# Optimization experiments

Hardware: AMD Instinct MI355X
Metric: run time of the kernel (lower is better)

## Reference

```python
import jax, jax.numpy as jnp
import numpy as np

B, N, F_IN, E, TOPK = 64, 1024, 64, 128, 32
NEG_SLOPE = 0.2  # GAT leaky-relu slope


def setup_inputs() -> dict:
    key = jax.random.key(0)
    ks = jax.random.split(key, 7)
    x = jax.random.normal(ks[0], (B, N, F_IN), dtype=jnp.float32)
    emb = jax.random.normal(ks[1], (N, E), dtype=jnp.float32)            # nn.Embedding table
    W_fe = jax.random.normal(ks[2], (F_IN, E), dtype=jnp.float32) / np.sqrt(F_IN).astype(np.float32)
    a_src = jax.random.normal(ks[3], (2 * E,), dtype=jnp.float32) * 0.05
    a_dst = jax.random.normal(ks[4], (2 * E,), dtype=jnp.float32) * 0.05
    lin_W = jax.random.normal(ks[5], (E, 1), dtype=jnp.float32) / np.sqrt(E).astype(np.float32)
    lin_b = jnp.zeros((1,), dtype=jnp.float32)
    return {"x": x, "emb": emb, "W_fe": W_fe, "a_src": a_src, "a_dst": a_dst,
            "lin_W": lin_W, "lin_b": lin_b}


def reference(x, emb, W_fe, a_src, a_dst, lin_W, lin_b):
    b, n, _ = x.shape
    e_dim = emb.shape[-1]
    # --- cosine-similarity topk graph construction (shared across batch) ---
    norm = jnp.linalg.norm(emb, axis=-1, keepdims=True)                  # [N,1]
    sim = (emb @ emb.T) / (norm @ norm.T)                                # [N,N]
    idx = jax.lax.top_k(sim, TOPK)[1]                                    # [N,K] int32 neighbor (target) nodes
    # --- graph attention feature extraction ---
    h = jnp.einsum('bnf,fe->bne', x, W_fe)                               # [B,N,E] projected node features
    g = jnp.concatenate([h, jnp.broadcast_to(emb, (b, n, e_dim))], -1)   # [B,N,2E] feat || embedding
    e_s = g @ a_src                                                      # [B,N] source attention term
    e_d = g @ a_dst                                                      # [B,N] target attention term
    # edges: source i repeated TOPK times -> targets idx[i]; softmax over each node's K neighbors
    scores = jax.nn.leaky_relu(e_s[:, :, None] + e_d[:, idx], NEG_SLOPE)  # [B,N,K]
    alpha = jax.nn.softmax(scores, axis=-1)                              # [B,N,K]
    h_dst = h[:, idx, :]                                                 # [B,N,K,E] gathered neighbor feats
    out = jnp.einsum('bnk,bnke->bne', alpha, h_dst)                      # aggregate messages
    out = jax.nn.relu(out)
    # --- linear readout ---
    y = out @ lin_W + lin_b                                              # [B,N,1]
    return y[..., 0]                                                     # [B,N]
```

## Files before the change

kernel.cpp:

```cpp
#include <hip/hip_runtime.h>
#include <math.h>

#define BB 64
#define NN 1024
#define F_IN 64
#define EE 128
#define TOPK 32
#define NEG_SLOPE 0.2f

typedef unsigned int uint;
typedef unsigned short ushort;
typedef unsigned long long ull;
typedef __attribute__((ext_vector_type(8))) short short8;
typedef __attribute__((ext_vector_type(4))) float f32x4;

static __device__ __forceinline__ uint f2bf(float f) {
  const uint x = __float_as_uint(f);
  return (x + 0x7fffu + ((x >> 16) & 1u)) >> 16;
}
static __device__ __forceinline__ float bf_lo(uint u) {
  return __uint_as_float(u << 16);
}
static __device__ __forceinline__ float bf_hi_raw(uint u) {
  return __uint_as_float(u);
}
static __device__ __forceinline__ uint fmono(float f) {
  uint u = __float_as_uint(f);
  return (u & 0x80000000u) ? ~u : (u | 0x80000000u);
}
static __device__ __forceinline__ ull umax64(ull a, ull b) {
  return a > b ? a : b;
}
static __device__ __forceinline__ ull umin64(ull a, ull b) {
  return a < b ? a : b;
}
static __device__ __forceinline__ ull shfl_xor64(ull v, int mask) {
  const uint lo = __shfl_xor((uint)v, mask);
  const uint hi = __shfl_xor((uint)(v >> 32), mask);
  return ((ull)hi << 32) | lo;
}

__global__ __launch_bounds__(256) void k2a_sim(
    const float* __restrict__ emb, const float* __restrict__ a_src,
    const float* __restrict__ a_dst, const float* __restrict__ W_fe,
    uint* __restrict__ keys, float* __restrict__ u_src,
    float* __restrict__ u_dst, ushort* __restrict__ wt) {
  __shared__ __align__(16) float ei[8][132];
  __shared__ __align__(16) float ej[64][132];
  const int t = threadIdx.x, wid = t >> 6, lane = t & 63;
  const int i0 = (blockIdx.x >> 2) * 8;
  const int jbase = (blockIdx.x & 3) * 256;

  if ((blockIdx.x & 3) == 0) {
    const int row = i0 + 2 * wid + (lane >> 5);
    const int ll = lane & 31;
    const float* er = emb + (size_t)row * EE;
    float us = 0.f, ud = 0.f;
#pragma unroll
    for (int c0 = 0; c0 < EE; c0 += 32) {
      const int c = c0 + ll;
      const float e = er[c];
      us += e * a_src[EE + c];
      ud += e * a_dst[EE + c];
    }
#pragma unroll
    for (int o = 1; o <= 16; o <<= 1) {
      us += __shfl_xor(us, o);
      ud += __shfl_xor(ud, o);
    }
    if (ll == 0) {
      u_src[row] = us;
      u_dst[row] = ud;
    }
  } else if ((blockIdx.x & 3) == 1 && (blockIdx.x >> 2) < 32) {
    const int g = (blockIdx.x >> 2) * 256 + t;
    const int n = g >> 6, k = g & 63;
    wt[g] = (ushort)f2bf(W_fe[k * EE + n]);
  }

  {
    const int r = t >> 5, c4 = t & 31;
    const float4 v = *(const float4*)&emb[(size_t)(i0 + r) * EE + c4 * 4];
    *(float4*)&ei[r][c4 * 4] = v;
  }

  const int ia = i0 + wid * 2;

  for (int ch = 0; ch < 4; ++ch) {
    const int j0 = jbase + ch * 64;
#pragma unroll
    for (int p = 0; p < 8; ++p) {
      const int g = p * 256 + t;
      const int r = g >> 5, c4 = g & 31;
      const float4 v = *(const float4*)&emb[(size_t)(j0 + r) * EE + c4 * 4];
      *(float4*)&ej[r][c4 * 4] = v;
    }
    __syncthreads();

    float a0 = 0.f, a1 = 0.f, sq = 0.f;
#pragma unroll 8
    for (int d4 = 0; d4 < 32; ++d4) {
      const float4 e = *(const float4*)&ej[lane][4 * d4];
      const float4 wa = *(const float4*)&ei[wid * 2][4 * d4];
      const float4 wb = *(const float4*)&ei[wid * 2 + 1][4 * d4];
      a0 += e.x * wa.x + e.y * wa.y + e.z * wa.z + e.w * wa.w;
      a1 += e.x * wb.x + e.y * wb.y + e.z * wb.z + e.w * wb.w;
      sq += e.x * e.x + e.y * e.y + e.z * e.z + e.w * e.w;
    }
    const int jg = j0 + lane;
    const float rj = rsqrtf(sq);
    keys[(size_t)ia * NN + jg] = fmono(a0 * rj);
    keys[(size_t)(ia + 1) * NN + jg] = fmono(a1 * rj);
    __syncthreads();
  }
}

__global__ __launch_bounds__(256) void k23(
    const uint* __restrict__ keys, int* __restrict__ idx_out,
    const float* __restrict__ x, const ushort* __restrict__ wt,
    const float* __restrict__ a_src, const float* __restrict__ a_dst,
    const float* __restrict__ u_src, const float* __restrict__ u_dst,
    uint* __restrict__ h2, float* __restrict__ es, float* __restrict__ ed) {
  __shared__ ull cand[128];
  const int t = threadIdx.x, wid = t >> 6, lane = t & 63;

  if (blockIdx.x < NN) {
    const int row = blockIdx.x;

    const int jb = wid * 256 + lane * 4;
    const uint4 kv = *(const uint4*)&keys[(size_t)row * NN + jb];
    ull xr[4];
    xr[0] = ((ull)kv.x << 32) | (uint)(jb + 0);
    xr[1] = ((ull)kv.y << 32) | (uint)(jb + 1);
    xr[2] = ((ull)kv.z << 32) | (uint)(jb + 2);
    xr[3] = ((ull)kv.w << 32) | (uint)(jb + 3);

#pragma unroll
    for (int k = 2; k <= 256; k <<= 1) {
#pragma unroll
      for (int d = 128; d >= 1; d >>= 1) {
        if (d > (k >> 1)) continue;
        if (d >= 4) {
          const int pl = d >> 2;
          const bool lower = (lane & pl) == 0;
#pragma unroll
          for (int r = 0; r < 4; ++r) {
            const ull o = shfl_xor64(xr[r], pl);
            const bool desc = (((lane * 4 + r) & k) == 0);
            const bool keepmax = (desc == lower);
            xr[r] = keepmax ? umax64(xr[r], o) : umin64(xr[r], o);
          }
        } else if (d == 2) {
#pragma unroll
          for (int r = 0; r < 2; ++r) {
            const bool desc = (((lane * 4 + r) & k) == 0);
            const ull hi = umax64(xr[r], xr[r + 2]);
            const ull lo = umin64(xr[r], xr[r + 2]);
            xr[r] = desc ? hi : lo;
            xr[r + 2] = desc ? lo : hi;
          }
        } else {
#pragma unroll
          for (int r = 0; r < 4; r += 2) {
            const bool desc = (((lane * 4 + r) & k) == 0);
            const ull hi = umax64(xr[r], xr[r + 1]);
            const ull lo = umin64(xr[r], xr[r + 1]);
            xr[r] = desc ? hi : lo;
            xr[r + 1] = desc ? lo : hi;
          }
        }
      }
    }
    if (lane < 8) {
#pragma unroll
      for (int r = 0; r < 4; ++r) cand[wid * 32 + lane * 4 + r] = xr[r];
    }
    __syncthreads();

    if (wid < 2) {
      const int base = wid * 64;
      ull v = (lane < 32) ? cand[base + lane] : cand[base + 95 - lane];
#pragma unroll
      for (int d = 32; d >= 1; d >>= 1) {
        const ull o = shfl_xor64(v, d);
        v = ((lane & d) == 0) ? umax64(v, o) : umin64(v, o);
      }
      if (lane < 32) cand[base + lane] = v;
    }
    __syncthreads();

    if (wid == 0) {
      ull v = (lane < 32) ? cand[lane] : cand[127 - lane];
#pragma unroll
      for (int d = 32; d >= 1; d >>= 1) {
        const ull o = shfl_xor64(v, d);
        v = ((lane & d) == 0) ? umax64(v, o) : umin64(v, o);
      }
      if (lane < 32) idx_out[(size_t)row * TOPK + lane] = (int)(v & 1023u);
    }
  } else {
    const int row0 = (blockIdx.x - NN) * 64;
    const int nn = lane & 15, quad = lane >> 4;
    const int row0w = row0 + wid * 16;

    short8 af[2];
#pragma unroll
    for (int s = 0; s < 2; ++s) {
      const float* xr2 = x + (size_t)(row0w + nn) * F_IN + s * 32 + quad * 8;
      const float4 v0 = *(const float4*)&xr2[0];
      const float4 v1 = *(const float4*)&xr2[4];
      af[s][0] = (short)f2bf(v0.x);
      af[s][1] = (short)f2bf(v0.y);
      af[s][2] = (short)f2bf(v0.z);
      af[s][3] = (short)f2bf(v0.w);
      af[s][4] = (short)f2bf(v1.x);
      af[s][5] = (short)f2bf(v1.y);
      af[s][6] = (short)f2bf(v1.z);
      af[s][7] = (short)f2bf(v1.w);
    }

    f32x4 acc[8];
#pragma unroll
    for (int T = 0; T < 8; ++T) acc[T] = (f32x4){0.f, 0.f, 0.f, 0.f};

#pragma unroll
    for (int T = 0; T < 8; ++T) {
#pragma unroll
      for (int s = 0; s < 2; ++s) {
        const short8 bf =
            *(const short8*)&wt[(T * 16 + nn) * F_IN + s * 32 + quad * 8];
        acc[T] =
            __builtin_amdgcn_mfma_f32_16x16x32_bf16(af[s], bf, acc[T], 0, 0, 0);
      }
    }

    const int growbase = row0w + quad * 4;
#pragma unroll
    for (int reg = 0; reg < 4; ++reg) {
      uint* hr = h2 + (size_t)(growbase + reg) * 64 + nn;
#pragma unroll
      for (int T4 = 0; T4 < 4; ++T4) {
        hr[T4 * 16] =
            f2bf(acc[2 * T4][reg]) | (f2bf(acc[2 * T4 + 1][reg]) << 16);
      }
    }
    float ae[8], de[8];
#pragma unroll
    for (int T = 0; T < 8; ++T) {
      ae[T] = a_src[T * 16 + nn];
      de[T] = a_dst[T * 16 + nn];
    }
#pragma unroll
    for (int reg = 0; reg < 4; ++reg) {
      float ps = 0.f, pd = 0.f;
#pragma unroll
      for (int T = 0; T < 8; ++T) {
        ps += acc[T][reg] * ae[T];
        pd += acc[T][reg] * de[T];
      }
#pragma unroll
      for (int o = 1; o <= 8; o <<= 1) {
        ps += __shfl_xor(ps, o);
        pd += __shfl_xor(pd, o);
      }
      if (nn == 0) {
        const int grow = growbase + reg;
        const int node = grow & (NN - 1);
        es[grow] = ps + u_src[node];
        ed[grow] = pd + u_dst[node];
      }
    }
  }
}

__global__ __launch_bounds__(256) void k4_attn(
    const uint* __restrict__ h2, const float* __restrict__ es,
    const float* __restrict__ ed, const int* __restrict__ idx,
    const float* __restrict__ lin_W, const float* __restrict__ lin_b,
    float* __restrict__ y) {
  const int t = threadIdx.x, wid = t >> 6, lane = t & 63;
  const int blk = blockIdx.x;
  const int xcd = blk & 7, x = blk >> 3;
  const int b = xcd * 8 + (x >> 6);
  const int q = lane >> 4, ll = lane & 15;
  const int n = (x & 63) * 16 + wid * 4 + q;
  const int pbase = q * 64;

  const float* edb = ed + (size_t)b * NN;
  const float* esb = es + (size_t)b * NN;
  const char* hb = (const char*)(h2 + (size_t)b * NN * 64);

  const int j0 = idx[n * TOPK + ll];
  const int j1 = idx[n * TOPK + 16 + ll];
  const int off0 = j0 << 8, off1 = j1 << 8;
  int offA[16], offB[16];
#pragma unroll
  for (int k = 0; k < 16; ++k) {
    offA[k] = __builtin_amdgcn_ds_bpermute(pbase + k * 4, off0);
    offB[k] = __builtin_amdgcn_ds_bpermute(pbase + k * 4, off1);
  }
  uint4 tvA[16];
#pragma unroll
  for (int k = 0; k < 16; ++k)
    tvA[k] = *(const uint4*)(hb + ((uint)offA[k] + ll * 16));
  uint4 tvB[16];
#pragma unroll
  for (int k = 0; k < 16; ++k)
    tvB[k] = *(const uint4*)(hb + ((uint)offB[k] + ll * 16));

  const float esv = esb[n];
  float s0 = esv + edb[j0];
  float s1 = esv + edb[j1];
  s0 = s0 > 0.f ? s0 : NEG_SLOPE * s0;
  s1 = s1 > 0.f ? s1 : NEG_SLOPE * s1;
  const float p0 = __expf(s0);
  const float p1 = __expf(s1);
  float dsum = p0 + p1;
#pragma unroll
  for (int o = 1; o <= 8; o <<= 1) dsum += __shfl_xor(dsum, o);
  const float rs = 1.0f / dsum;
  const float w0 = p0 * rs, w1 = p1 * rs;
  float wkA[16], wkB[16];
#pragma unroll
  for (int k = 0; k < 16; ++k) {
    wkA[k] = __uint_as_float(
        __builtin_amdgcn_ds_bpermute(pbase + k * 4, __float_as_uint(w0)));
    wkB[k] = __uint_as_float(
        __builtin_amdgcn_ds_bpermute(pbase + k * 4, __float_as_uint(w1)));
  }

  float lwlo[4], lwhi[4];
#pragma unroll
  for (int i = 0; i < 4; ++i) {
    const int c = 4 * ll + i;
    const int t4 = c >> 4, nn2 = c & 15;
    lwlo[i] = lin_W[t4 * 32 + nn2];
    lwhi[i] = lin_W[t4 * 32 + 16 + nn2];
  }
  const float bias = lin_b[0];

  float acc[8];
#pragma unroll
  for (int i = 0; i < 8; i++) acc[i] = 0.f;
#pragma unroll
  for (int k = 0; k < 16; ++k) {
    const float ak = wkA[k];
    const uint4 u = tvA[k];
    acc[0] += ak * bf_lo(u.x);
    acc[1] += ak * bf_hi_raw(u.x);
    acc[2] += ak * bf_lo(u.y);
    acc[3] += ak * bf_hi_raw(u.y);
    acc[4] += ak * bf_lo(u.z);
    acc[5] += ak * bf_hi_raw(u.z);
    acc[6] += ak * bf_lo(u.w);
    acc[7] += ak * bf_hi_raw(u.w);
  }
#pragma unroll
  for (int k = 0; k < 16; ++k) {
    const float ak = wkB[k];
    const uint4 u = tvB[k];
    acc[0] += ak * bf_lo(u.x);
    acc[1] += ak * bf_hi_raw(u.x);
    acc[2] += ak * bf_lo(u.y);
    acc[3] += ak * bf_hi_raw(u.y);
    acc[4] += ak * bf_lo(u.z);
    acc[5] += ak * bf_hi_raw(u.z);
    acc[6] += ak * bf_lo(u.w);
    acc[7] += ak * bf_hi_raw(u.w);
  }
  float r = 0.f;
#pragma unroll
  for (int i = 0; i < 4; ++i) {
    const float a0 = acc[2 * i] > 0.f ? acc[2 * i] : 0.f;
    const float a1 = acc[2 * i + 1] > 0.f ? acc[2 * i + 1] : 0.f;
    r += a0 * lwlo[i] + a1 * lwhi[i];
  }
#pragma unroll
  for (int o = 1; o <= 8; o <<= 1) r += __shfl_xor(r, o);
  if (ll == 0) y[(size_t)b * NN + n] = r + bias;
}

extern "C" void kernel_launch(void* const* d_in, const int* in_sizes, int n_in,
                              void* d_out, int out_size, void* d_ws,
                              size_t ws_size, hipStream_t stream) {
  const float* x = (const float*)d_in[0];
  const float* emb = (const float*)d_in[1];
  const float* W_fe = (const float*)d_in[2];
  const float* a_src = (const float*)d_in[3];
  const float* a_dst = (const float*)d_in[4];
  const float* lin_W = (const float*)d_in[5];
  const float* lin_b = (const float*)d_in[6];
  float* y = (float*)d_out;

  char* ws = (char*)d_ws;
  float* u_src = (float*)(ws + 4096);
  float* u_dst = (float*)(ws + 8192);
  int* idx = (int*)(ws + 16384);
  float* es = (float*)(ws + 147456);
  float* ed = (float*)(ws + 409600);
  uint* h2 = (uint*)(ws + 671744);
  uint* keys = (uint*)(ws + 17448960);
  ushort* wt = (ushort*)(ws + 21643264);

  k2a_sim<<<512, 256, 0, stream>>>(emb, a_src, a_dst, W_fe, keys, u_src,
                                   u_dst, wt);
  k23<<<2048, 256, 0, stream>>>(keys, idx, x, wt, a_src, a_dst, u_src, u_dst,
                                h2, es, ed);
  k4_attn<<<4096, 256, 0, stream>>>(h2, es, ed, idx, lin_W, lin_b, y);
}
```

Before: 131.2 us.

## Stage neighbor offsets/weights in LDS and double-buffer gathers in attention kernel

Replaces the ds_bpermute broadcast of neighbor offsets and softmax weights with a per-node LDS staging array holding (offset, unnormalized exp) pairs. The 32 neighbor-row gathers are split into four groups of eight and double-buffered so loads overlap the FMA accumulation. Softmax normalization is deferred: the exp sum is accumulated in the loop and applied once after ReLU and the readout dot product, which is valid because the scale is positive. It also adds a launch_bounds occupancy hint of 3 blocks, cutting register pressure from 32 live uint4 values to 16. The LDS writes and reads happen within the same wavefront with no explicit barrier, which relies on in-order wave execution.

```diff
diff --git a/kernel.cpp b/kernel.cpp
--- a/kernel.cpp
+++ b/kernel.cpp
@@ -273,61 +273,39 @@
   }
 }
 
-__global__ __launch_bounds__(256) void k4_attn(
+__global__ __launch_bounds__(256, 3) void k4_attn(
     const uint* __restrict__ h2, const float* __restrict__ es,
     const float* __restrict__ ed, const int* __restrict__ idx,
     const float* __restrict__ lin_W, const float* __restrict__ lin_b,
     float* __restrict__ y) {
+  __shared__ uint2 pairs[16 * 34 + 2];
   const int t = threadIdx.x, wid = t >> 6, lane = t & 63;
   const int blk = blockIdx.x;
-  const int xcd = blk & 7, x = blk >> 3;
-  const int b = xcd * 8 + (x >> 6);
+  const int xcd = blk & 7, xx = blk >> 3;
+  const int b = xcd * 8 + (xx >> 6);
   const int q = lane >> 4, ll = lane & 15;
-  const int n = (x & 63) * 16 + wid * 4 + q;
-  const int pbase = q * 64;
+  const int n = (xx & 63) * 16 + wid * 4 + q;
+  uint2* const pr = pairs + (wid * 4 + q) * 34;
 
   const float* edb = ed + (size_t)b * NN;
-  const float* esb = es + (size_t)b * NN;
   const char* hb = (const char*)(h2 + (size_t)b * NN * 64);
 
   const int j0 = idx[n * TOPK + ll];
   const int j1 = idx[n * TOPK + 16 + ll];
-  const int off0 = j0 << 8, off1 = j1 << 8;
-  int offA[16], offB[16];
-#pragma unroll
-  for (int k = 0; k < 16; ++k) {
-    offA[k] = __builtin_amdgcn_ds_bpermute(pbase + k * 4, off0);
-    offB[k] = __builtin_amdgcn_ds_bpermute(pbase + k * 4, off1);
-  }
-  uint4 tvA[16];
-#pragma unroll
-  for (int k = 0; k < 16; ++k)
-    tvA[k] = *(const uint4*)(hb + ((uint)offA[k] + ll * 16));
-  uint4 tvB[16];
-#pragma unroll
-  for (int k = 0; k < 16; ++k)
-    tvB[k] = *(const uint4*)(hb + ((uint)offB[k] + ll * 16));
-
-  const float esv = esb[n];
+  const float esv = es[(size_t)b * NN + n];
   float s0 = esv + edb[j0];
   float s1 = esv + edb[j1];
   s0 = s0 > 0.f ? s0 : NEG_SLOPE * s0;
   s1 = s1 > 0.f ? s1 : NEG_SLOPE * s1;
   const float p0 = __expf(s0);
   const float p1 = __expf(s1);
-  float dsum = p0 + p1;
-#pragma unroll
-  for (int o = 1; o <= 8; o <<= 1) dsum += __shfl_xor(dsum, o);
-  const float rs = 1.0f / dsum;
-  const float w0 = p0 * rs, w1 = p1 * rs;
-  float wkA[16], wkB[16];
-#pragma unroll
-  for (int k = 0; k < 16; ++k) {
-    wkA[k] = __uint_as_float(
-        __builtin_amdgcn_ds_bpermute(pbase + k * 4, __float_as_uint(w0)));
-    wkB[k] = __uint_as_float(
-        __builtin_amdgcn_ds_bpermute(pbase + k * 4, __float_as_uint(w1)));
-  }
+  uint2 st0, st1;
+  st0.x = (uint)(j0 << 8);
+  st0.y = __float_as_uint(p0);
+  st1.x = (uint)(j1 << 8);
+  st1.y = __float_as_uint(p1);
+  pr[ll] = st0;
+  pr[16 + ll] = st1;
 
   float lwlo[4], lwhi[4];
 #pragma unroll
@@ -339,35 +317,50 @@
   }
   const float bias = lin_b[0];
 
+  float w[32];
   float acc[8];
 #pragma unroll
-  for (int i = 0; i < 8; i++) acc[i] = 0.f;
-#pragma unroll
-  for (int k = 0; k < 16; ++k) {
-    const float ak = wkA[k];
-    const uint4 u = tvA[k];
-    acc[0] += ak * bf_lo(u.x);
-    acc[1] += ak * bf_hi_raw(u.x);
-    acc[2] += ak * bf_lo(u.y);
-    acc[3] += ak * bf_hi_raw(u.y);
-    acc[4] += ak * bf_lo(u.z);
-    acc[5] += ak * bf_hi_raw(u.z);
-    acc[6] += ak * bf_lo(u.w);
-    acc[7] += ak * bf_hi_raw(u.w);
-  }
-#pragma unroll
-  for (int k = 0; k < 16; ++k) {
-    const float ak = wkB[k];
-    const uint4 u = tvB[k];
-    acc[0] += ak * bf_lo(u.x);
-    acc[1] += ak * bf_hi_raw(u.x);
-    acc[2] += ak * bf_lo(u.y);
-    acc[3] += ak * bf_hi_raw(u.y);
-    acc[4] += ak * bf_lo(u.z);
-    acc[5] += ak * bf_hi_raw(u.z);
-    acc[6] += ak * bf_lo(u.w);
-    acc[7] += ak * bf_hi_raw(u.w);
-  }
+  for (int i = 0; i < 8; ++i) acc[i] = 0.f;
+  float dsum = 0.f;
+  uint4 tvA[8], tvB[8];
+
+#define LOADG(g, TV)                                                \
+  {                                                                 \
+    _Pragma("unroll") for (int k = 0; k < 8; ++k) {                 \
+      const uint2 pw = pr[(g) * 8 + k];                             \
+      w[(g) * 8 + k] = __uint_as_float(pw.y);                       \
+      TV[k] = *(const uint4*)(hb + (pw.x + (uint)(ll * 16)));       \
+    }                                                               \
+  }
+#define CONSG(g, TV)                                \
+  {                                                 \
+    _Pragma("unroll") for (int k = 0; k < 8; ++k) { \
+      const float wk = w[(g) * 8 + k];              \
+      dsum += wk;                                   \
+      const uint4 u = TV[k];                        \
+      acc[0] += wk * bf_lo(u.x);                    \
+      acc[1] += wk * bf_hi_raw(u.x);                \
+      acc[2] += wk * bf_lo(u.y);                    \
+      acc[3] += wk * bf_hi_raw(u.y);                \
+      acc[4] += wk * bf_lo(u.z);                    \
+      acc[5] += wk * bf_hi_raw(u.z);                \
+      acc[6] += wk * bf_lo(u.w);                    \
+      acc[7] += wk * bf_hi_raw(u.w);                \
+    }                                               \
+  }
+
+  LOADG(0, tvA)
+  LOADG(1, tvB)
+  CONSG(0, tvA)
+  LOADG(2, tvA)
+  CONSG(1, tvB)
+  LOADG(3, tvB)
+  CONSG(2, tvA)
+  CONSG(3, tvB)
+#undef LOADG
+#undef CONSG
+
+  const float rs = 1.0f / dsum;
   float r = 0.f;
 #pragma unroll
   for (int i = 0; i < 4; ++i) {
@@ -377,7 +370,7 @@
   }
 #pragma unroll
   for (int o = 1; o <= 8; o <<= 1) r += __shfl_xor(r, o);
-  if (ll == 0) y[(size_t)b * NN + n] = r + bias;
+  if (ll == 0) y[(size_t)b * NN + n] = r * rs + bias;
 }
 
 extern "C" void kernel_launch(void* const* d_in, const int* in_sizes, int n_in,
```

New measurement: 148.0 us. 1.13x slower.

## Compute cosine similarity with bf16 MFMA and refine top-k candidates in fp32

Applied to the files above, without the earlier changes.

The similarity kernel now normalises the embedding rows, converts them to bf16 in swizzled shared memory, and computes the 1024x1024 similarity matrix with 16x16x32 bf16 MFMA instructions instead of fp32 scalar dot products. The grid drops from 512 to 256 blocks, and each block now tiles 16 rows by 256 columns. Because bf16 keys can reorder near-ties, the top-k kernel keeps 64 candidates per row instead of 32. It recomputes their cosine in fp32 using the stored reciprocal norms, then bitonic-sorts them to pick the final 32. This trades extra gather and sort work in the top-k kernel for a cheaper matrix product, at some risk of missing a true neighbour ranked beyond 64 by bf16.

```diff
diff --git a/kernel.cpp b/kernel.cpp
--- a/kernel.cpp
+++ b/kernel.cpp
@@ -44,74 +44,125 @@
     const float* __restrict__ emb, const float* __restrict__ a_src,
     const float* __restrict__ a_dst, const float* __restrict__ W_fe,
     uint* __restrict__ keys, float* __restrict__ u_src,
-    float* __restrict__ u_dst, ushort* __restrict__ wt) {
-  __shared__ __align__(16) float ei[8][132];
-  __shared__ __align__(16) float ej[64][132];
+    float* __restrict__ u_dst, ushort* __restrict__ wt,
+    float* __restrict__ rn) {
+  __shared__ __align__(16) uint eni[16 * 64];
+  __shared__ __align__(16) uint enj[256 * 64];
   const int t = threadIdx.x, wid = t >> 6, lane = t & 63;
-  const int i0 = (blockIdx.x >> 2) * 8;
-  const int jbase = (blockIdx.x & 3) * 256;
-
-  if ((blockIdx.x & 3) == 0) {
-    const int row = i0 + 2 * wid + (lane >> 5);
-    const int ll = lane & 31;
-    const float* er = emb + (size_t)row * EE;
-    float us = 0.f, ud = 0.f;
-#pragma unroll
-    for (int c0 = 0; c0 < EE; c0 += 32) {
-      const int c = c0 + ll;
-      const float e = er[c];
-      us += e * a_src[EE + c];
-      ud += e * a_dst[EE + c];
-    }
-#pragma unroll
-    for (int o = 1; o <= 16; o <<= 1) {
-      us += __shfl_xor(us, o);
-      ud += __shfl_xor(ud, o);
-    }
-    if (ll == 0) {
-      u_src[row] = us;
-      u_dst[row] = ud;
-    }
-  } else if ((blockIdx.x & 3) == 1 && (blockIdx.x >> 2) < 32) {
-    const int g = (blockIdx.x >> 2) * 256 + t;
+  const int it = blockIdx.x >> 2, js = blockIdx.x & 3;
+  const int i0 = it * 16, jw0 = js * 256;
+
+  const int rh = t >> 1, h = t & 1;
+#pragma unroll
+  for (int p = 0; p < 2; ++p) {
+    const int r = p * 128 + rh;
+    const float* src = emb + (size_t)(jw0 + r) * EE + h * 64;
+    float4 v[16];
+#pragma unroll
+    for (int q = 0; q < 16; ++q) v[q] = *(const float4*)&src[q * 4];
+    float sq = 0.f;
+#pragma unroll
+    for (int q = 0; q < 16; ++q)
+      sq += v[q].x * v[q].x + v[q].y * v[q].y + v[q].z * v[q].z +
+            v[q].w * v[q].w;
+    sq += __shfl_xor(sq, 1);
+    const float rs = rsqrtf(sq);
+    if (it == 0 && h == 0) rn[jw0 + r] = rs;
+    char* dst = (char*)(enj + r * 64);
+    const int swz = (r & 7) << 4;
+#pragma unroll
+    for (int s16 = 0; s16 < 8; ++s16) {
+      const float4 a = v[s16 * 2], b2 = v[s16 * 2 + 1];
+      uint4 w4;
+      w4.x = f2bf(a.x * rs) | (f2bf(a.y * rs) << 16);
+      w4.y = f2bf(a.z * rs) | (f2bf(a.w * rs) << 16);
+      w4.z = f2bf(b2.x * rs) | (f2bf(b2.y * rs) << 16);
+      w4.w = f2bf(b2.z * rs) | (f2bf(b2.w * rs) << 16);
+      *(uint4*)(dst + ((h * 128 + s16 * 16) ^ swz)) = w4;
+    }
+  }
+  if (t < 32) {
+    const int r = t >> 1, hh = t & 1;
+    const float* src = emb + (size_t)(i0 + r) * EE + hh * 64;
+    float4 v[16];
+#pragma unroll
+    for (int q = 0; q < 16; ++q) v[q] = *(const float4*)&src[q * 4];
+    float sq = 0.f;
+#pragma unroll
+    for (int q = 0; q < 16; ++q)
+      sq += v[q].x * v[q].x + v[q].y * v[q].y + v[q].z * v[q].z +
+            v[q].w * v[q].w;
+    sq += __shfl_xor(sq, 1);
+    const float rs = rsqrtf(sq);
+    char* dst = (char*)(eni + r * 64);
+    const int swz = (r & 7) << 4;
+#pragma unroll
+    for (int s16 = 0; s16 < 8; ++s16) {
+      const float4 a = v[s16 * 2], b2 = v[s16 * 2 + 1];
+      uint4 w4;
+      w4.x = f2bf(a.x * rs) | (f2bf(a.y * rs) << 16);
+      w4.y = f2bf(a.z * rs) | (f2bf(a.w * rs) << 16);
+      w4.z = f2bf(b2.x * rs) | (f2bf(b2.y * rs) << 16);
+      w4.w = f2bf(b2.z * rs) | (f2bf(b2.w * rs) << 16);
+      *(uint4*)(dst + ((hh * 128 + s16 * 16) ^ swz)) = w4;
+    }
+  }
+  __syncthreads();
+
+  const int nn = lane & 15, quad = lane >> 4;
+  short8 af[4];
+#pragma unroll
+  for (int s = 0; s < 4; ++s) {
+    const int kb = (s * 64 + quad * 16) ^ ((nn & 7) << 4);
+    af[s] = *(const short8*)((const char*)eni + nn * 256 + kb);
+  }
+  f32x4 acc[4];
+#pragma unroll
+  for (int t4 = 0; t4 < 4; ++t4) acc[t4] = (f32x4){0.f, 0.f, 0.f, 0.f};
+#pragma unroll
+  for (int t4 = 0; t4 < 4; ++t4) {
+    const int rloc = wid * 64 + t4 * 16 + nn;
+    const char* brow = (const char*)enj + rloc * 256;
+    const int swz = (rloc & 7) << 4;
+#pragma unroll
+    for (int s = 0; s < 4; ++s) {
+      const short8 bf = *(const short8*)(brow + ((s * 64 + quad * 16) ^ swz));
+      acc[t4] =
+          __builtin_amdgcn_mfma_f32_16x16x32_bf16(af[s], bf, acc[t4], 0, 0, 0);
+    }
+  }
+#pragma unroll
+  for (int t4 = 0; t4 < 4; ++t4) {
+    const int j = jw0 + wid * 64 + t4 * 16 + nn;
+#pragma unroll
+    for (int reg = 0; reg < 4; ++reg) {
+      const int i = i0 + quad * 4 + reg;
+      keys[(size_t)i * NN + j] = fmono(acc[t4][reg]);
+    }
+  }
+
+  if (js == 0) {
+#pragma unroll
+    for (int rr = 0; rr < 4; ++rr) {
+      const int row = i0 + wid * 4 + rr;
+      const float* er = emb + (size_t)row * EE;
+      const float e0 = er[lane], e1 = er[64 + lane];
+      float us = e0 * a_src[EE + lane] + e1 * a_src[EE + 64 + lane];
+      float ud = e0 * a_dst[EE + lane] + e1 * a_dst[EE + 64 + lane];
+#pragma unroll
+      for (int o = 1; o <= 32; o <<= 1) {
+        us += __shfl_xor(us, o);
+        ud += __shfl_xor(ud, o);
+      }
+      if (lane == 0) {
+        u_src[row] = us;
+        u_dst[row] = ud;
+      }
+    }
+  } else if (js == 1 && it < 32) {
+    const int g = it * 256 + t;
     const int n = g >> 6, k = g & 63;
     wt[g] = (ushort)f2bf(W_fe[k * EE + n]);
-  }
-
-  {
-    const int r = t >> 5, c4 = t & 31;
-    const float4 v = *(const float4*)&emb[(size_t)(i0 + r) * EE + c4 * 4];
-    *(float4*)&ei[r][c4 * 4] = v;
-  }
-
-  const int ia = i0 + wid * 2;
-
-  for (int ch = 0; ch < 4; ++ch) {
-    const int j0 = jbase + ch * 64;
-#pragma unroll
-    for (int p = 0; p < 8; ++p) {
-      const int g = p * 256 + t;
-      const int r = g >> 5, c4 = g & 31;
-      const float4 v = *(const float4*)&emb[(size_t)(j0 + r) * EE + c4 * 4];
-      *(float4*)&ej[r][c4 * 4] = v;
-    }
-    __syncthreads();
-
-    float a0 = 0.f, a1 = 0.f, sq = 0.f;
-#pragma unroll 8
-    for (int d4 = 0; d4 < 32; ++d4) {
-      const float4 e = *(const float4*)&ej[lane][4 * d4];
-      const float4 wa = *(const float4*)&ei[wid * 2][4 * d4];
-      const float4 wb = *(const float4*)&ei[wid * 2 + 1][4 * d4];
-      a0 += e.x * wa.x + e.y * wa.y + e.z * wa.z + e.w * wa.w;
-      a1 += e.x * wb.x + e.y * wb.y + e.z * wb.z + e.w * wb.w;
-      sq += e.x * e.x + e.y * e.y + e.z * e.z + e.w * e.w;
-    }
-    const int jg = j0 + lane;
-    const float rj = rsqrtf(sq);
-    keys[(size_t)ia * NN + jg] = fmono(a0 * rj);
-    keys[(size_t)(ia + 1) * NN + jg] = fmono(a1 * rj);
-    __syncthreads();
   }
 }
 
@@ -120,12 +171,15 @@
     const float* __restrict__ x, const ushort* __restrict__ wt,
     const float* __restrict__ a_src, const float* __restrict__ a_dst,
     const float* __restrict__ u_src, const float* __restrict__ u_dst,
-    uint* __restrict__ h2, float* __restrict__ es, float* __restrict__ ed) {
-  __shared__ ull cand[128];
+    uint* __restrict__ h2, float* __restrict__ es, float* __restrict__ ed,
+    const float* __restrict__ emb, const float* __restrict__ rn) {
+  __shared__ ull cand[256];
+  __shared__ float rowbuf[EE];
   const int t = threadIdx.x, wid = t >> 6, lane = t & 63;
 
   if (blockIdx.x < NN) {
     const int row = blockIdx.x;
+    if (t < EE) rowbuf[t] = emb[(size_t)row * EE + t];
 
     const int jb = wid * 256 + lane * 4;
     const uint4 kv = *(const uint4*)&keys[(size_t)row * NN + jb];
@@ -171,30 +225,68 @@
         }
       }
     }
-    if (lane < 8) {
-#pragma unroll
-      for (int r = 0; r < 4; ++r) cand[wid * 32 + lane * 4 + r] = xr[r];
+    if (lane < 16) {
+#pragma unroll
+      for (int r = 0; r < 4; ++r) cand[wid * 64 + lane * 4 + r] = xr[r];
     }
     __syncthreads();
 
     if (wid < 2) {
-      const int base = wid * 64;
-      ull v = (lane < 32) ? cand[base + lane] : cand[base + 95 - lane];
+      const ull a0 = cand[(2 * wid) * 64 + lane];
+      const ull a1 = cand[(2 * wid) * 64 + 64 + 63 - lane];
+      ull v0 = umax64(a0, a1);
 #pragma unroll
       for (int d = 32; d >= 1; d >>= 1) {
-        const ull o = shfl_xor64(v, d);
-        v = ((lane & d) == 0) ? umax64(v, o) : umin64(v, o);
-      }
-      if (lane < 32) cand[base + lane] = v;
+        const ull o = shfl_xor64(v0, d);
+        v0 = ((lane & d) == 0) ? umax64(v0, o) : umin64(v0, o);
+      }
+      cand[wid * 128 + lane] = v0;
     }
     __syncthreads();
 
     if (wid == 0) {
-      ull v = (lane < 32) ? cand[lane] : cand[127 - lane];
+      const ull a0 = cand[lane];
+      const ull a1 = cand[128 + 63 - lane];
+      ull v0 = umax64(a0, a1);
 #pragma unroll
       for (int d = 32; d >= 1; d >>= 1) {
-        const ull o = shfl_xor64(v, d);
-        v = ((lane & d) == 0) ? umax64(v, o) : umin64(v, o);
+        const ull o = shfl_xor64(v0, d);
+        v0 = ((lane & d) == 0) ? umax64(v0, o) : umin64(v0, o);
+      }
+      cand[192 + lane] = v0 & 1023u;
+    }
+    __syncthreads();
+
+    const int c = t >> 2, dq = t & 3;
+    const int jc = (int)(uint)cand[192 + c];
+    const float* ej = emb + (size_t)jc * EE + dq * 32;
+    const float* rb = rowbuf + dq * 32;
+    float dot = 0.f;
+#pragma unroll
+    for (int q = 0; q < 8; ++q) {
+      const float4 a = *(const float4*)&ej[q * 4];
+      const float4 b = *(const float4*)&rb[q * 4];
+      dot += a.x * b.x + a.y * b.y + a.z * b.z + a.w * b.w;
+    }
+    dot += __shfl_xor(dot, 1);
+    dot += __shfl_xor(dot, 2);
+    if (dq == 0) {
+      const float cosv = dot * rn[row] * rn[jc];
+      cand[c] = ((ull)fmono(cosv) << 32) | (uint)jc;
+    }
+    __syncthreads();
+
+    if (wid == 0) {
+      ull v = cand[lane];
+#pragma unroll
+      for (int k = 2; k <= 64; k <<= 1) {
+#pragma unroll
+        for (int d0 = 32; d0 >= 1; d0 >>= 1) {
+          if (d0 > (k >> 1)) continue;
+          const ull o = shfl_xor64(v, d0);
+          const bool up = (lane & k) == 0;
+          v = (up == ((lane & d0) == 0)) ? umax64(v, o) : umin64(v, o);
+        }
       }
       if (lane < 32) idx_out[(size_t)row * TOPK + lane] = (int)(v & 1023u);
     }
@@ -393,6 +485,7 @@
   float* y = (float*)d_out;
 
   char* ws = (char*)d_ws;
+  float* rn = (float*)(ws + 0);
   float* u_src = (float*)(ws + 4096);
   float* u_dst = (float*)(ws + 8192);
   int* idx = (int*)(ws + 16384);
@@ -402,9 +495,9 @@
   uint* keys = (uint*)(ws + 17448960);
   ushort* wt = (ushort*)(ws + 21643264);
 
-  k2a_sim<<<512, 256, 0, stream>>>(emb, a_src, a_dst, W_fe, keys, u_src,
-                                   u_dst, wt);
+  k2a_sim<<<256, 256, 0, stream>>>(emb, a_src, a_dst, W_fe, keys, u_src,
+                                   u_dst, wt, rn);
   k23<<<2048, 256, 0, stream>>>(keys, idx, x, wt, a_src, a_dst, u_src, u_dst,
-                                h2, es, ed);
+                                h2, es, ed, emb, rn);
   k4_attn<<<4096, 256, 0, stream>>>(h2, es, ed, idx, lin_W, lin_b, y);
 }
```

New measurement: 128.8 us. No clear change (-1.8%).
